# Performance work log

Hardware: AMD Instinct MI355X
Metric: run time of the kernel (lower is better)

## Reference

```python
import jax, jax.numpy as jnp
import numpy as np

H = 1024
NUM_HEADS = 16
E = 4
I = H * 4 // E  # expert intermediate size = 1024
EPS = 1e-6


def layer_norm(x, g, b):
    mu = jnp.mean(x, axis=-1, keepdims=True)
    var = jnp.mean(jnp.square(x - mu), axis=-1, keepdims=True)
    return (x - mu) * jax.lax.rsqrt(var + EPS) * g + b


def setup_inputs() -> dict:
    key = jax.random.key(0)
    ks = jax.random.split(key, 12)
    B, Nq, Nkv = 4, 1024, 2048
    inp = {
        "query": jax.random.normal(ks[0], (B, Nq, H), jnp.float32),
        "key_value": jax.random.normal(ks[1], (B, Nkv, H), jnp.float32),
        "Wq": jax.random.normal(ks[2], (H, H), jnp.float32) * 0.02,
        "bq": jnp.zeros((H,), jnp.float32),
        "Wk": jax.random.normal(ks[3], (H, H), jnp.float32) * 0.02,
        "bk": jnp.zeros((H,), jnp.float32),
        "Wv": jax.random.normal(ks[4], (H, H), jnp.float32) * 0.02,
        "bv": jnp.zeros((H,), jnp.float32),
        "Wo": jax.random.normal(ks[5], (H, H), jnp.float32) * 0.02,
        "bo": jnp.zeros((H,), jnp.float32),
        "g1": jnp.ones((H,), jnp.float32),
        "b1": jnp.zeros((H,), jnp.float32),
        "g2": jnp.ones((H,), jnp.float32),
        "b2": jnp.zeros((H,), jnp.float32),
        "gate_up": jax.random.normal(ks[6], (E, H, 2 * I), jnp.float32) * 0.02,
        "down": jax.random.normal(ks[7], (E, I, H), jnp.float32) * 0.02,
    }
    return inp


def reference(query, key_value, Wq, bq, Wk, bk, Wv, bv, Wo, bo,
              g1, b1, g2, b2, gate_up, down):
    B, Nq, _ = query.shape
    Nkv = key_value.shape[1]
    d = H // NUM_HEADS
    scale = d ** -0.5

    # ---- cross-attention with pre-norm + residual ----
    x = layer_norm(query, g1, b1)
    q = (x @ Wq + bq).reshape(B, Nq, NUM_HEADS, d)
    k = (key_value @ Wk + bk).reshape(B, Nkv, NUM_HEADS, d)
    v = (key_value @ Wv + bv).reshape(B, Nkv, NUM_HEADS, d)
    scores = jnp.einsum("bqhd,bkhd->bhqk", q, k) * scale
    attn = jax.nn.softmax(scores, axis=-1)
    ctx = jnp.einsum("bhqk,bkhd->bqhd", attn, v).reshape(B, Nq, H)
    x = query + (ctx @ Wo + bo)

    # ---- token-routed MoE SwiGLU MLP (expert = pos % E) ----
    residual = x
    h = layer_norm(x, g2, b2)
    outs = []
    for e in range(E):
        xe = h[:, e::E]                      # [B, Nq/E, H] tokens routed to expert e
        gu = xe @ gate_up[e]                 # [B, Nq/E, 2I]
        gate, up = gu[..., :I], gu[..., I:]
        inter = jax.nn.silu(gate) * up
        outs.append(inter @ down[e])         # [B, Nq/E, H]
    moe = jnp.stack(outs, axis=2).reshape(B, Nq, H)  # interleave back to position order
    return residual + moe
```

## Files before the change

kernel.cpp:

```cpp
#include <hip/hip_runtime.h>
#include <hip/hip_bf16.h>

typedef unsigned short u16;
typedef float f32x4 __attribute__((ext_vector_type(4)));
typedef short s16x8 __attribute__((ext_vector_type(8)));

__device__ __forceinline__ u16 f2b(float f) {
    union { float f; unsigned u; } c; c.f = f;
    unsigned r = c.u + 0x7fffu + ((c.u >> 16) & 1u);
    return (u16)(r >> 16);
}
__device__ __forceinline__ unsigned pkbf16(float a, float b) {
    union { __hip_bfloat162 h; unsigned u; } c;
    c.h = __float22bfloat162_rn(float2{a, b});
    return c.u;
}

#define ASYNC_COPY16(gp, lp)                                                       \
    __builtin_amdgcn_global_load_lds(                                              \
        (const __attribute__((address_space(1))) void*)(gp),                       \
        (__attribute__((address_space(3))) void*)(lp), 16, 0, 0)

__device__ __forceinline__ void transcast_body(const float* __restrict__ Wz,
                                               u16* __restrict__ Wtz,
                                               int K, int N, int bx, int by,
                                               int permute) {
    __shared__ float tile[64][65];
    const int n0 = bx * 64, k0 = by * 64;
    const int tid = threadIdx.x;
    const int tx = tid & 15, ty = tid >> 4;
#pragma unroll
    for (int it = 0; it < 4; it++) {
        int r = ty + it * 16;
        float4 v = *(const float4*)&Wz[(size_t)(k0 + r) * N + n0 + tx * 4];
        tile[r][tx * 4 + 0] = v.x;
        tile[r][tx * 4 + 1] = v.y;
        tile[r][tx * 4 + 2] = v.z;
        tile[r][tx * 4 + 3] = v.w;
    }
    __syncthreads();
    int n = tid >> 2;
    int ks = (tid & 3) * 16;
    int drow = n0 + n;
    if (permute) drow = (drow < 1024) ? 2 * drow : 2 * (drow - 1024) + 1;
    u16* dst = &Wtz[(size_t)drow * K + k0 + ks];
#pragma unroll
    for (int h = 0; h < 2; h++) {
        uint4 o;
        o.x = pkbf16(tile[ks + h * 8 + 0][n], tile[ks + h * 8 + 1][n]);
        o.y = pkbf16(tile[ks + h * 8 + 2][n], tile[ks + h * 8 + 3][n]);
        o.z = pkbf16(tile[ks + h * 8 + 4][n], tile[ks + h * 8 + 5][n]);
        o.w = pkbf16(tile[ks + h * 8 + 6][n], tile[ks + h * 8 + 7][n]);
        *(uint4*)(dst + h * 8) = o;
    }
}

__global__ __launch_bounds__(256) void transcast64(const float* __restrict__ W,
                                                   u16* __restrict__ Wt,
                                                   int K, int N, long long zstride,
                                                   int permute) {
    transcast_body(W + (size_t)blockIdx.z * zstride, Wt + (size_t)blockIdx.z * zstride,
                   K, N, blockIdx.x, blockIdx.y, permute);
}

__global__ __launch_bounds__(256) void transcast4(
    const float* __restrict__ W0, const float* __restrict__ W1,
    const float* __restrict__ W2, const float* __restrict__ W3,
    u16* __restrict__ O0, u16* __restrict__ O1,
    u16* __restrict__ O2, u16* __restrict__ O3) {
    const int z = blockIdx.z;
    const float* W = (z == 0) ? W0 : (z == 1) ? W1 : (z == 2) ? W2 : W3;
    u16* O = (z == 0) ? O0 : (z == 1) ? O1 : (z == 2) ? O2 : O3;
    transcast_body(W, O, 1024, 1024, blockIdx.x, blockIdx.y, 0);
}

__global__ __launch_bounds__(256) void cast_kernel(const float* __restrict__ x,
                                                   u16* __restrict__ y, int n8) {
    int id = blockIdx.x * 256 + threadIdx.x;
    if (id >= n8) return;
    const float* p = x + (size_t)id * 8;
    float4 a = *(const float4*)p;
    float4 b = *(const float4*)(p + 4);
    uint4 o;
    o.x = pkbf16(a.x, a.y);
    o.y = pkbf16(a.z, a.w);
    o.z = pkbf16(b.x, b.y);
    o.w = pkbf16(b.z, b.w);
    *(uint4*)(y + (size_t)id * 8) = o;
}

__global__ __launch_bounds__(256) void ln_kernel(const float* __restrict__ x,
                                                 const float* __restrict__ g,
                                                 const float* __restrict__ bb,
                                                 u16* __restrict__ out, int pack) {
    int token = blockIdx.x;
    int tid = threadIdx.x;
    const float* row = x + (size_t)token * 1024;
    float4 v = *(const float4*)(row + tid * 4);
    float s1 = v.x + v.y + v.z + v.w;
    float s2 = v.x * v.x + v.y * v.y + v.z * v.z + v.w * v.w;
#pragma unroll
    for (int off = 32; off > 0; off >>= 1) {
        s1 += __shfl_down(s1, off);
        s2 += __shfl_down(s2, off);
    }
    __shared__ float ws1[4], ws2[4];
    int wave = tid >> 6;
    if ((tid & 63) == 0) { ws1[wave] = s1; ws2[wave] = s2; }
    __syncthreads();
    float t1 = ws1[0] + ws1[1] + ws1[2] + ws1[3];
    float t2 = ws2[0] + ws2[1] + ws2[2] + ws2[3];
    float mean = t1 * (1.f / 1024.f);
    float var = t2 * (1.f / 1024.f) - mean * mean;
    float rstd = rsqrtf(var + 1e-6f);
    size_t dest = token;
    if (pack) {
        int bq = token >> 10, q = token & 1023;
        dest = (size_t)(q & 3) * 1024 + (size_t)bq * 256 + (q >> 2);
    }
    int c = tid * 4;
    float4 gv = *(const float4*)(g + c);
    float4 bv = *(const float4*)(bb + c);
    uint2 o;
    o.x = pkbf16((v.x - mean) * rstd * gv.x + bv.x, (v.y - mean) * rstd * gv.y + bv.y);
    o.y = pkbf16((v.z - mean) * rstd * gv.z + bv.z, (v.w - mean) * rstd * gv.w + bv.w);
    *(uint2*)&out[dest * 1024 + c] = o;
}

template <int BM>
__global__ __launch_bounds__(256) void gemm_t(
    const u16* __restrict__ A, const u16* __restrict__ Bt,
    const float* __restrict__ bias0, const float* __restrict__ bias1, int biasSplit,
    const float* __restrict__ resid,
    float* __restrict__ outF, u16* __restrict__ outH,
    int M, int N, int K,
    long long aStride, long long bStride, long long oStride,
    int mode, float outScale) {
    constexpr int NJ = (BM == 128) ? 4 : 2;
    __shared__ __align__(16) u16 As[BM * 64];
    __shared__ __align__(16) u16 Bs[128 * 64];
    const int z = blockIdx.z;
    const u16* Ab = A + (size_t)z * aStride;
    const u16* Bb = Bt + (size_t)z * bStride;
    const int m0 = blockIdx.y * BM, n0 = blockIdx.x * 128;
    const int tid = threadIdx.x;
    const int wave = tid >> 6, lane = tid & 63;
    const int wm = (BM == 128) ? (wave >> 1) * 64 : 0;
    const int wn = (BM == 128) ? (wave & 1) * 64 : wave * 32;
    const int quad = lane >> 4, l16 = lane & 15;
    f32x4 acc[4][NJ] = {};
    for (int k0 = 0; k0 < K; k0 += 64) {
#pragma unroll
        for (int i = 0; i < BM / 32; i++) {
            int id = tid + i * 256;
            int row = id >> 3, c = id & 7;
            int srcseg = c ^ (row & 7);
            ASYNC_COPY16(&Ab[(size_t)(m0 + row) * K + k0 + srcseg * 8],
                         As + (size_t)(wave * 64 + i * 256) * 8);
        }
#pragma unroll
        for (int i = 0; i < 4; i++) {
            int id = tid + i * 256;
            int row = id >> 3, c = id & 7;
            int srcseg = c ^ (row & 7);
            ASYNC_COPY16(&Bb[(size_t)(n0 + row) * K + k0 + srcseg * 8],
                         Bs + (size_t)(wave * 64 + i * 256) * 8);
        }
        __syncthreads();
#pragma unroll
        for (int kk = 0; kk < 2; kk++) {
            s16x8 af[4], bfr[NJ];
#pragma unroll
            for (int i = 0; i < 4; i++) {
                int row = wm + i * 16 + l16;
                af[i] = *(const s16x8*)&As[row * 64 + ((kk * 4 + quad) ^ (row & 7)) * 8];
            }
#pragma unroll
            for (int j = 0; j < NJ; j++) {
                int row = wn + j * 16 + l16;
                bfr[j] = *(const s16x8*)&Bs[row * 64 + ((kk * 4 + quad) ^ (row & 7)) * 8];
            }
#pragma unroll
            for (int i = 0; i < 4; i++)
#pragma unroll
                for (int j = 0; j < NJ; j++)
                    acc[i][j] = __builtin_amdgcn_mfma_f32_16x16x32_bf16(af[i], bfr[j], acc[i][j], 0, 0, 0);
        }
        __syncthreads();
    }
#pragma unroll
    for (int i = 0; i < 4; i++) {
#pragma unroll
        for (int j = 0; j < NJ; j++) {
            int col = n0 + wn + j * 16 + l16;
            float bv = 0.f;
            if (bias0) bv = (col < biasSplit) ? bias0[col] : bias1[col - biasSplit];
#pragma unroll
            for (int r = 0; r < 4; r++) {
                int row = m0 + wm + i * 16 + quad * 4 + r;
                float v = acc[i][j][r] + bv;
                if (mode == 2) {
                    float other = __shfl_xor(v, 1);
                    if (!(lane & 1)) {
                        float res = (v / (1.f + __expf(-v))) * other;
                        outH[(size_t)z * oStride + (size_t)row * (N >> 1) + (col >> 1)] = f2b(res);
                    }
                } else if (mode == 1) {
                    int bb2 = row >> 8, qi = row & 255;
                    size_t oidx = ((size_t)bb2 * 1024 + (size_t)z + 4 * (size_t)qi) * N + col;
                    outF[oidx] = v + resid[oidx];
                } else {
                    size_t oidx = (size_t)z * oStride + (size_t)row * N + col;
                    if (resid) v += resid[oidx];
                    if (outF) outF[oidx] = v;
                    else outH[oidx] = f2b(v * outScale);
                }
            }
        }
    }
}

__global__ __launch_bounds__(256) void flash_attn(
    const u16* __restrict__ Q, const u16* __restrict__ KV, u16* __restrict__ O) {
    const int lidx = blockIdx.x;
    const int xcd = lidx & 7, slot = lidx >> 3;
    const int g = xcd + 8 * (slot >> 4);
    const int qt = slot & 15;
    const int b = g >> 4, h = g & 15;
    const int tid = threadIdx.x, wave = tid >> 6, lane = tid & 63;
    const int quad = lane >> 4, l16 = lane & 15;
    const int q0 = qt * 64 + wave * 16;

    __shared__ __align__(16) u16 Ks[64 * 64];
    __shared__ __align__(16) u16 Vt[64 * 64];
    __shared__ __align__(16) unsigned Pt[4][16 * 36];

    const size_t qrow = ((size_t)b * 1024 + q0 + l16) * 1024 + (size_t)h * 64;
    s16x8 qf0 = *(const s16x8*)&Q[qrow + quad * 8];
    s16x8 qf1 = *(const s16x8*)&Q[qrow + 32 + quad * 8];

    f32x4 o[4] = {};
    float l = 0.f;

    const u16* Kbh = KV + ((size_t)b * 2048) * 2048 + (size_t)h * 64;
    const u16* Vbh = Kbh + 1024;

    const int kp = tid >> 3;
    const int dg = tid & 7;
    const int vswz = ((dg & 1) << 4) | ((dg >> 1) << 2);
    unsigned* Vtd = (unsigned*)Vt;
    const uint4* Ks128 = (const uint4*)Ks;

    for (int kc = 0; kc < 2048; kc += 64) {
        __syncthreads();
#pragma unroll
        for (int i = 0; i < 2; i++) {
            int id = tid + i * 256;
            int row = id >> 3;
            int srcseg = (id & 7) ^ (row & 7);
            ASYNC_COPY16(Kbh + (size_t)(kc + row) * 2048 + srcseg * 8,
                         &Ks[(size_t)(wave * 64 + i * 256) * 8]);
        }
        {
            const u16* va = Vbh + (size_t)(kc + 2 * kp) * 2048 + dg * 8;
            uint4 A_ = *(const uint4*)va;
            uint4 B_ = *(const uint4*)(va + 2048);
            int colp = kp ^ vswz;
            unsigned* vd = &Vtd[dg * 8 * 32 + colp];
            vd[0 * 32] = __builtin_amdgcn_perm(B_.x, A_.x, 0x05040100u);
            vd[1 * 32] = __builtin_amdgcn_perm(B_.x, A_.x, 0x07060302u);
            vd[2 * 32] = __builtin_amdgcn_perm(B_.y, A_.y, 0x05040100u);
            vd[3 * 32] = __builtin_amdgcn_perm(B_.y, A_.y, 0x07060302u);
            vd[4 * 32] = __builtin_amdgcn_perm(B_.z, A_.z, 0x05040100u);
            vd[5 * 32] = __builtin_amdgcn_perm(B_.z, A_.z, 0x07060302u);
            vd[6 * 32] = __builtin_amdgcn_perm(B_.w, A_.w, 0x05040100u);
            vd[7 * 32] = __builtin_amdgcn_perm(B_.w, A_.w, 0x07060302u);
        }
        __syncthreads();

        f32x4 s[4];
#pragma unroll
        for (int kt = 0; kt < 4; kt++) {
            int row = kt * 16 + l16;
            union { uint4 v; s16x8 f; } a0, a1;
            a0.v = Ks128[row * 8 + (quad ^ (row & 7))];
            a1.v = Ks128[row * 8 + ((4 + quad) ^ (row & 7))];
            f32x4 acc = {};
            acc = __builtin_amdgcn_mfma_f32_16x16x32_bf16(a0.f, qf0, acc, 0, 0, 0);
            acc = __builtin_amdgcn_mfma_f32_16x16x32_bf16(a1.f, qf1, acc, 0, 0, 0);
            s[kt] = acc;
        }

        float p[16], rs = 0.f;
#pragma unroll
        for (int kt = 0; kt < 4; kt++)
#pragma unroll
            for (int r = 0; r < 4; r++) {
                float e = __expf(s[kt][r] - 4.0f);
                p[kt * 4 + r] = e;
                rs += e;
            }
        rs += __shfl_xor(rs, 16);
        rs += __shfl_xor(rs, 32);
        l += rs;

        unsigned* pw = &Pt[wave][l16 * 36];
#pragma unroll
        for (int kt = 0; kt < 4; kt++) {
            uint2 dw;
            dw.x = pkbf16(p[kt * 4 + 0], p[kt * 4 + 1]);
            dw.y = pkbf16(p[kt * 4 + 2], p[kt * 4 + 3]);
            *(uint2*)&pw[kt * 8 + quad * 2] = dw;
        }
        asm volatile("s_waitcnt lgkmcnt(0)" ::: "memory");

#pragma unroll
        for (int c = 0; c < 2; c++) {
            union { uint4 v; s16x8 f; } pf;
            pf.v = *(const uint4*)&Pt[wave][l16 * 36 + c * 16 + quad * 4];
#pragma unroll
            for (int dt = 0; dt < 4; dt++) {
                int d = 16 * dt + l16;
                int colp = (c * 16 + quad * 4) ^ (((l16 >> 3) << 4) | ((dt & 3) << 2));
                union { uint4 v; s16x8 f; } vf;
                vf.v = *(const uint4*)&Vtd[d * 32 + colp];
                o[dt] = __builtin_amdgcn_mfma_f32_16x16x32_bf16(vf.f, pf.f, o[dt], 0, 0, 0);
            }
        }
    }

    float inv = 1.f / l;
    size_t orow = ((size_t)b * 1024 + q0 + l16) * 1024 + (size_t)h * 64;
#pragma unroll
    for (int dt = 0; dt < 4; dt++) {
        uint2 dw;
        dw.x = pkbf16(o[dt][0] * inv, o[dt][1] * inv);
        dw.y = pkbf16(o[dt][2] * inv, o[dt][3] * inv);
        *(uint2*)&O[orow + dt * 16 + quad * 4] = dw;
    }
}

extern "C" void kernel_launch(void* const* d_in, const int* in_sizes, int n_in,
                              void* d_out, int out_size, void* d_ws, size_t ws_size,
                              hipStream_t stream) {
    (void)in_sizes; (void)n_in; (void)out_size; (void)ws_size;
    const float* query     = (const float*)d_in[0];
    const float* key_value = (const float*)d_in[1];
    const float* Wq = (const float*)d_in[2];
    const float* bq = (const float*)d_in[3];
    const float* Wk = (const float*)d_in[4];
    const float* bk = (const float*)d_in[5];
    const float* Wv = (const float*)d_in[6];
    const float* bv = (const float*)d_in[7];
    const float* Wo = (const float*)d_in[8];
    const float* bo = (const float*)d_in[9];
    const float* g1 = (const float*)d_in[10];
    const float* b1 = (const float*)d_in[11];
    const float* g2 = (const float*)d_in[12];
    const float* b2 = (const float*)d_in[13];
    const float* gate_up = (const float*)d_in[14];
    const float* down    = (const float*)d_in[15];
    float* out = (float*)d_out;

    char* wsb = (char*)d_ws;
    size_t off = 0;
    auto alloc = [&](size_t bytes) {
        char* p = wsb + off;
        off += (bytes + 255) & ~(size_t)255;
        return (void*)p;
    };
    u16* buf8a = (u16*)alloc((size_t)4096 * 1024 * 2);
    u16* qb    = (u16*)alloc((size_t)4096 * 1024 * 2);
    u16* kvb   = (u16*)alloc((size_t)8192 * 2048 * 2);
    u16* kvbf  = (u16*)alloc((size_t)8192 * 1024 * 2);
    float* x2  = (float*)alloc((size_t)4096 * 1024 * 4);
    u16* wqt   = (u16*)alloc((size_t)1024 * 1024 * 2);
    u16* kvw   = (u16*)alloc((size_t)2048 * 1024 * 2);
    u16* wot   = (u16*)alloc((size_t)1024 * 1024 * 2);
    u16* gut   = (u16*)alloc((size_t)4 * 2048 * 1024 * 2);
    u16* dnt   = (u16*)alloc((size_t)4 * 1024 * 1024 * 2);
    u16* xn = buf8a; u16* ctx = buf8a; u16* hp = buf8a;
    u16* inter = kvbf;
    const int BIG = 1 << 30;

    transcast4<<<dim3(16, 16, 4), 256, 0, stream>>>(
        Wq, Wk, Wv, Wo, wqt, kvw, kvw + (size_t)1024 * 1024, wot);
    transcast64<<<dim3(32, 16, 4), 256, 0, stream>>>(gate_up, gut, 1024, 2048, (long long)1024 * 2048, 1);
    transcast64<<<dim3(16, 16, 4), 256, 0, stream>>>(down, dnt, 1024, 1024, (long long)1024 * 1024, 0);
    cast_kernel<<<4096, 256, 0, stream>>>(key_value, kvbf, 1048576);
    ln_kernel<<<4096, 256, 0, stream>>>(query, g1, b1, xn, 0);
    gemm_t<64><<<dim3(8, 64, 1), 256, 0, stream>>>(xn, wqt, bq, bq, BIG, nullptr, nullptr, qb,
        4096, 1024, 1024, 0, 0, 0, 0, 0.125f);
    gemm_t<128><<<dim3(16, 64, 1), 256, 0, stream>>>(kvbf, kvw, bk, bv, 1024, nullptr, nullptr, kvb,
        8192, 2048, 1024, 0, 0, 0, 0, 1.f);
    flash_attn<<<1024, 256, 0, stream>>>(qb, kvb, ctx);
    gemm_t<64><<<dim3(8, 64, 1), 256, 0, stream>>>(ctx, wot, bo, bo, BIG, query, x2, nullptr,
        4096, 1024, 1024, 0, 0, 0, 0, 1.f);
    ln_kernel<<<4096, 256, 0, stream>>>(x2, g2, b2, hp, 1);
    gemm_t<64><<<dim3(16, 16, 4), 256, 0, stream>>>(hp, gut, nullptr, nullptr, BIG, nullptr, nullptr, inter,
        1024, 2048, 1024,
        (long long)1024 * 1024, (long long)2048 * 1024, (long long)1024 * 1024, 2, 1.f);
    gemm_t<64><<<dim3(8, 16, 4), 256, 0, stream>>>(inter, dnt, nullptr, nullptr, BIG, x2, out, nullptr,
        1024, 1024, 1024,
        (long long)1024 * 1024, (long long)1024 * 1024, 0, 1, 1.f);
}
```

Before: 431.2 us.

## Write V pre-transposed from KV GEMM epilogue and async-load it in attention

The KV projection GEMM gains an epilogue mode that writes K row-major and V transposed per head into separate buffers. Flash attention then loads V tiles with async global-to-LDS copies instead of register loads plus perm-based transposition into LDS. The softmax scaling is folded into the Q projection with log2(e), so the kernel uses exp2f with a constant offset. The transposed V stores in the GEMM epilogue are narrow 8-byte scattered writes, which may cost some GEMM store efficiency.

```diff
diff --git a/kernel.cpp b/kernel.cpp
--- a/kernel.cpp
+++ b/kernel.cpp
@@ -132,7 +132,7 @@
     const u16* __restrict__ A, const u16* __restrict__ Bt,
     const float* __restrict__ bias0, const float* __restrict__ bias1, int biasSplit,
     const float* __restrict__ resid,
-    float* __restrict__ outF, u16* __restrict__ outH,
+    float* __restrict__ outF, u16* __restrict__ outH, u16* __restrict__ outH2,
     int M, int N, int K,
     long long aStride, long long bStride, long long oStride,
     int mode, float outScale) {
@@ -195,6 +195,25 @@
             int col = n0 + wn + j * 16 + l16;
             float bv = 0.f;
             if (bias0) bv = (col < biasSplit) ? bias0[col] : bias1[col - biasSplit];
+            if (mode == 3) {
+                float vr[4];
+#pragma unroll
+                for (int r = 0; r < 4; r++) vr[r] = acc[i][j][r] + bv;
+                int row0 = m0 + wm + i * 16 + quad * 4;
+                if (col < 1024) {
+#pragma unroll
+                    for (int r = 0; r < 4; r++)
+                        outH[(size_t)(row0 + r) * 1024 + col] = f2b(vr[r]);
+                } else {
+                    int bb2 = row0 >> 11, key = row0 & 2047;
+                    int hh = (col - 1024) >> 6, d = (col - 1024) & 63;
+                    uint2 dw;
+                    dw.x = pkbf16(vr[0], vr[1]);
+                    dw.y = pkbf16(vr[2], vr[3]);
+                    *(uint2*)&outH2[(((size_t)bb2 * 16 + hh) * 64 + d) * 2048 + key] = dw;
+                }
+                continue;
+            }
 #pragma unroll
             for (int r = 0; r < 4; r++) {
                 int row = m0 + wm + i * 16 + quad * 4 + r;
@@ -221,7 +240,8 @@
 }
 
 __global__ __launch_bounds__(256) void flash_attn(
-    const u16* __restrict__ Q, const u16* __restrict__ KV, u16* __restrict__ O) {
+    const u16* __restrict__ Q, const u16* __restrict__ Kb,
+    const u16* __restrict__ VT, u16* __restrict__ O) {
     const int lidx = blockIdx.x;
     const int xcd = lidx & 7, slot = lidx >> 3;
     const int g = xcd + 8 * (slot >> 4);
@@ -232,7 +252,7 @@
     const int q0 = qt * 64 + wave * 16;
 
     __shared__ __align__(16) u16 Ks[64 * 64];
-    __shared__ __align__(16) u16 Vt[64 * 64];
+    __shared__ __align__(16) u16 Vs[64 * 64];
     __shared__ __align__(16) unsigned Pt[4][16 * 36];
 
     const size_t qrow = ((size_t)b * 1024 + q0 + l16) * 1024 + (size_t)h * 64;
@@ -241,15 +261,12 @@
 
     f32x4 o[4] = {};
     float l = 0.f;
-
-    const u16* Kbh = KV + ((size_t)b * 2048) * 2048 + (size_t)h * 64;
-    const u16* Vbh = Kbh + 1024;
-
-    const int kp = tid >> 3;
-    const int dg = tid & 7;
-    const int vswz = ((dg & 1) << 4) | ((dg >> 1) << 2);
-    unsigned* Vtd = (unsigned*)Vt;
+    const float C2 = 5.770780163555852f;
+
+    const u16* Kbh = Kb + ((size_t)b * 2048) * 1024 + (size_t)h * 64;
+    const u16* VTbh = VT + (((size_t)b * 16 + h) * 64) * 2048;
     const uint4* Ks128 = (const uint4*)Ks;
+    const uint4* Vs128 = (const uint4*)Vs;
 
     for (int kc = 0; kc < 2048; kc += 64) {
         __syncthreads();
@@ -258,23 +275,16 @@
             int id = tid + i * 256;
             int row = id >> 3;
             int srcseg = (id & 7) ^ (row & 7);
-            ASYNC_COPY16(Kbh + (size_t)(kc + row) * 2048 + srcseg * 8,
+            ASYNC_COPY16(Kbh + (size_t)(kc + row) * 1024 + srcseg * 8,
                          &Ks[(size_t)(wave * 64 + i * 256) * 8]);
         }
-        {
-            const u16* va = Vbh + (size_t)(kc + 2 * kp) * 2048 + dg * 8;
-            uint4 A_ = *(const uint4*)va;
-            uint4 B_ = *(const uint4*)(va + 2048);
-            int colp = kp ^ vswz;
-            unsigned* vd = &Vtd[dg * 8 * 32 + colp];
-            vd[0 * 32] = __builtin_amdgcn_perm(B_.x, A_.x, 0x05040100u);
-            vd[1 * 32] = __builtin_amdgcn_perm(B_.x, A_.x, 0x07060302u);
-            vd[2 * 32] = __builtin_amdgcn_perm(B_.y, A_.y, 0x05040100u);
-            vd[3 * 32] = __builtin_amdgcn_perm(B_.y, A_.y, 0x07060302u);
-            vd[4 * 32] = __builtin_amdgcn_perm(B_.z, A_.z, 0x05040100u);
-            vd[5 * 32] = __builtin_amdgcn_perm(B_.z, A_.z, 0x07060302u);
-            vd[6 * 32] = __builtin_amdgcn_perm(B_.w, A_.w, 0x05040100u);
-            vd[7 * 32] = __builtin_amdgcn_perm(B_.w, A_.w, 0x07060302u);
+#pragma unroll
+        for (int i = 0; i < 2; i++) {
+            int id = tid + i * 256;
+            int row = id >> 3;
+            int srcseg = (id & 7) ^ (row & 7);
+            ASYNC_COPY16(VTbh + (size_t)row * 2048 + kc + srcseg * 8,
+                         &Vs[(size_t)(wave * 64 + i * 256) * 8]);
         }
         __syncthreads();
 
@@ -296,7 +306,7 @@
         for (int kt = 0; kt < 4; kt++)
 #pragma unroll
             for (int r = 0; r < 4; r++) {
-                float e = __expf(s[kt][r] - 4.0f);
+                float e = exp2f(s[kt][r] - C2);
                 p[kt * 4 + r] = e;
                 rs += e;
             }
@@ -320,10 +330,9 @@
             pf.v = *(const uint4*)&Pt[wave][l16 * 36 + c * 16 + quad * 4];
 #pragma unroll
             for (int dt = 0; dt < 4; dt++) {
-                int d = 16 * dt + l16;
-                int colp = (c * 16 + quad * 4) ^ (((l16 >> 3) << 4) | ((dt & 3) << 2));
+                int row = dt * 16 + l16;
                 union { uint4 v; s16x8 f; } vf;
-                vf.v = *(const uint4*)&Vtd[d * 32 + colp];
+                vf.v = Vs128[row * 8 + ((c * 4 + quad) ^ (row & 7))];
                 o[dt] = __builtin_amdgcn_mfma_f32_16x16x32_bf16(vf.f, pf.f, o[dt], 0, 0, 0);
             }
         }
@@ -371,7 +380,8 @@
     };
     u16* buf8a = (u16*)alloc((size_t)4096 * 1024 * 2);
     u16* qb    = (u16*)alloc((size_t)4096 * 1024 * 2);
-    u16* kvb   = (u16*)alloc((size_t)8192 * 2048 * 2);
+    u16* kvb   = (u16*)alloc((size_t)8192 * 1024 * 2);
+    u16* vtb   = (u16*)alloc((size_t)8192 * 1024 * 2);
     u16* kvbf  = (u16*)alloc((size_t)8192 * 1024 * 2);
     float* x2  = (float*)alloc((size_t)4096 * 1024 * 4);
     u16* wqt   = (u16*)alloc((size_t)1024 * 1024 * 2);
@@ -382,6 +392,7 @@
     u16* xn = buf8a; u16* ctx = buf8a; u16* hp = buf8a;
     u16* inter = kvbf;
     const int BIG = 1 << 30;
+    const float QSCALE = 0.125f * 1.44269504f;
 
     transcast4<<<dim3(16, 16, 4), 256, 0, stream>>>(
         Wq, Wk, Wv, Wo, wqt, kvw, kvw + (size_t)1024 * 1024, wot);
@@ -389,18 +400,18 @@
     transcast64<<<dim3(16, 16, 4), 256, 0, stream>>>(down, dnt, 1024, 1024, (long long)1024 * 1024, 0);
     cast_kernel<<<4096, 256, 0, stream>>>(key_value, kvbf, 1048576);
     ln_kernel<<<4096, 256, 0, stream>>>(query, g1, b1, xn, 0);
-    gemm_t<64><<<dim3(8, 64, 1), 256, 0, stream>>>(xn, wqt, bq, bq, BIG, nullptr, nullptr, qb,
-        4096, 1024, 1024, 0, 0, 0, 0, 0.125f);
-    gemm_t<128><<<dim3(16, 64, 1), 256, 0, stream>>>(kvbf, kvw, bk, bv, 1024, nullptr, nullptr, kvb,
-        8192, 2048, 1024, 0, 0, 0, 0, 1.f);
-    flash_attn<<<1024, 256, 0, stream>>>(qb, kvb, ctx);
-    gemm_t<64><<<dim3(8, 64, 1), 256, 0, stream>>>(ctx, wot, bo, bo, BIG, query, x2, nullptr,
+    gemm_t<64><<<dim3(8, 64, 1), 256, 0, stream>>>(xn, wqt, bq, bq, BIG, nullptr, nullptr, qb, nullptr,
+        4096, 1024, 1024, 0, 0, 0, 0, QSCALE);
+    gemm_t<128><<<dim3(16, 64, 1), 256, 0, stream>>>(kvbf, kvw, bk, bv, 1024, nullptr, nullptr, kvb, vtb,
+        8192, 2048, 1024, 0, 0, 0, 3, 1.f);
+    flash_attn<<<1024, 256, 0, stream>>>(qb, kvb, vtb, ctx);
+    gemm_t<64><<<dim3(8, 64, 1), 256, 0, stream>>>(ctx, wot, bo, bo, BIG, query, x2, nullptr, nullptr,
         4096, 1024, 1024, 0, 0, 0, 0, 1.f);
     ln_kernel<<<4096, 256, 0, stream>>>(x2, g2, b2, hp, 1);
-    gemm_t<64><<<dim3(16, 16, 4), 256, 0, stream>>>(hp, gut, nullptr, nullptr, BIG, nullptr, nullptr, inter,
+    gemm_t<64><<<dim3(16, 16, 4), 256, 0, stream>>>(hp, gut, nullptr, nullptr, BIG, nullptr, nullptr, inter, nullptr,
         1024, 2048, 1024,
         (long long)1024 * 1024, (long long)2048 * 1024, (long long)1024 * 1024, 2, 1.f);
-    gemm_t<64><<<dim3(8, 16, 4), 256, 0, stream>>>(inter, dnt, nullptr, nullptr, BIG, x2, out, nullptr,
+    gemm_t<64><<<dim3(8, 16, 4), 256, 0, stream>>>(inter, dnt, nullptr, nullptr, BIG, x2, out, nullptr, nullptr,
         1024, 1024, 1024,
         (long long)1024 * 1024, (long long)1024 * 1024, 0, 1, 1.f);
 }
```

After: 423.4 us. About the same (-1.8%).
